# Kernel tuning notes

Measured on AMD Instinct MI355X. Metric: run time of the kernel, lower is better.

Reference implementation:

```python
import jax, jax.numpy as jnp
import numpy as np

C, A, K, S = 128, 64, 24, 4           # molecules, atoms, neighbors, species
RCR, RCA = 5.2, 3.5                   # radial / angular cutoffs (Angstrom)
ETA_R, ETA_A, ZETA = 16.0, 8.0, 32.0
LAYERS = [384, 160, 128, 96, 1]       # per-element MLP
NPAIR = S * (S + 1) // 2              # 10 unordered species pairs

_triu = np.zeros((S, S), np.int32)
_c = 0
for _i in range(S):
    for _j in range(_i, S):
        _triu[_i, _j] = _triu[_j, _i] = _c
        _c += 1
TRIU = jnp.asarray(_triu)
JJ, KK = np.triu_indices(K, 1)        # static pair-of-neighbors indices, T = K(K-1)/2


def setup_inputs() -> dict:
    key = jax.random.key(0)
    ks = jax.random.split(key, 12)
    element_idxs = jax.random.randint(ks[0], (C, A), 0, S, dtype=jnp.int32)
    neighbor_idxs = jax.random.randint(ks[1], (C, A, K), 0, A, dtype=jnp.int32)
    distances = jax.random.uniform(ks[2], (C, A, K), minval=0.8, maxval=5.0, dtype=jnp.float32)
    dirs = jax.random.normal(ks[3], (C, A, K, 3), dtype=jnp.float32)
    dirs = dirs / jnp.linalg.norm(dirs, axis=-1, keepdims=True)
    diff_vectors = dirs * distances[..., None]
    inp = {"element_idxs": element_idxs, "neighbor_idxs": neighbor_idxs,
           "distances": distances, "diff_vectors": diff_vectors}
    k = 4
    for i, (fin, fout) in enumerate(zip(LAYERS[:-1], LAYERS[1:]), 1):
        inp[f"W{i}"] = jax.random.normal(ks[k], (S, fin, fout), dtype=jnp.float32) / np.sqrt(fin).astype(np.float32); k += 1
        inp[f"b{i}"] = jax.random.normal(ks[k], (S, fout), dtype=jnp.float32) * 0.01; k += 1
    return inp


def _fc(d, rc):
    # smooth cosine cutoff, exactly zero beyond rc
    return jnp.where(d < rc, 0.5 * jnp.cos(np.float32(np.pi) * d / rc) + 0.5, 0.0)


def _celu(x, a=0.1):
    return jnp.where(x > 0, x, a * jnp.expm1(x / a))


def reference(element_idxs, neighbor_idxs, distances, diff_vectors,
              W1, b1, W2, b2, W3, b3, W4, b4):
    shfr = jnp.linspace(0.9, RCR, 17, dtype=jnp.float32)[:-1]                 # (16,)
    shfa = jnp.linspace(0.9, RCA, 5, dtype=jnp.float32)[:-1]                  # (4,)
    shfz = (jnp.arange(8, dtype=jnp.float32) + 0.5) * np.float32(np.pi / 8)   # (8,)

    # species of each neighbor: (C,A,K)
    nspec = element_idxs[jnp.arange(C)[:, None, None], neighbor_idxs]

    # ---- radial sub-AEV: (C,A,S,16) ----
    fcr = _fc(distances, RCR)
    rterm = 0.25 * jnp.exp(-ETA_R * (distances[..., None] - shfr) ** 2) * fcr[..., None]  # (C,A,K,16)
    oh_s = jax.nn.one_hot(nspec, S, dtype=rterm.dtype)                                     # (C,A,K,S)
    radial = jnp.einsum('cakr,caks->casr', rterm, oh_s).reshape(C, A, S * 16)

    # ---- angular sub-AEV over neighbor pairs (j<k): T = K(K-1)/2 ----
    d1, d2 = distances[..., JJ], distances[..., KK]                 # (C,A,T)
    v1, v2 = diff_vectors[..., JJ, :], diff_vectors[..., KK, :]      # (C,A,T,3)
    cosang = jnp.sum(v1 * v2, axis=-1) / (d1 * d2)
    ang = jnp.arccos(0.95 * cosang)                                  # torchani's 0.95 nan-guard
    f1 = ((1.0 + jnp.cos(ang[..., None] - shfz)) * 0.5) ** ZETA      # (C,A,T,8)
    f2 = jnp.exp(-ETA_A * ((d1 + d2) * 0.5)[..., None] - shfa * 0.0) if False else \
         jnp.exp(-ETA_A * (((d1 + d2) * 0.5)[..., None] - shfa) ** 2)  # (C,A,T,4)
    fc12 = _fc(d1, RCA) * _fc(d2, RCA)                               # (C,A,T)
    aterm = (2.0 * f1[..., :, None] * f2[..., None, :] * fc12[..., None, None]).reshape(C, A, JJ.size, 32)
    pidx = TRIU[nspec[..., JJ], nspec[..., KK]]                      # (C,A,T) in [0,10)
    oh_p = jax.nn.one_hot(pidx, NPAIR, dtype=aterm.dtype)            # (C,A,T,10)
    angular = jnp.einsum('catf,catp->capf', aterm, oh_p).reshape(C, A, NPAIR * 32)

    aev = jnp.concatenate([radial, angular], axis=-1)                # (C,A,384)

    # ---- per-element MLPs (computed for all species, then gathered) ----
    h = _celu(jnp.einsum('caf,sfo->caso', aev, W1) + b1)
    h = _celu(jnp.einsum('casf,sfo->caso', h, W2) + b2)
    h = _celu(jnp.einsum('casf,sfo->caso', h, W3) + b3)
    out = (jnp.einsum('casf,sfo->caso', h, W4) + b4)[..., 0]         # (C,A,S)
    atomic = jnp.take_along_axis(out, element_idxs[..., None], axis=2)[..., 0]  # (C,A)
    return atomic.sum(axis=-1)                                       # (C,) molecular energies
```

## Files before the change

kernel.cpp:

```cpp
#include <hip/hip_runtime.h>
#include <math.h>

constexpr int C_ = 128, A_ = 64, K_ = 24, S_ = 4;
constexpr int NATOM = C_ * A_;
constexpr int FAEV = 384;
constexpr float RCR = 5.2f, RCA = 3.5f;
constexpr float PI_F = 3.14159265358979323846f;
constexpr float K_A2 = -8.0f  * 1.44269504f;
constexpr float K_R2 = -64.0f * 1.44269504f;
constexpr float SQRT095 = 0.974679434f;
constexpr float SQRT2   = 1.41421356237f;

__global__ __launch_bounds__(256) void aev_kernel(const int* __restrict__ element_idxs,
                                                  const int* __restrict__ neighbor_idxs,
                                                  const float* __restrict__ distances,
                                                  const float* __restrict__ diff_vectors,
                                                  float* __restrict__ aev_out,
                                                  int* __restrict__ mol_cnt,
                                                  int* __restrict__ mol_lst,
                                                  float* __restrict__ out) {
    const int blk = blockIdx.x;
    const int c   = blk >> 4;
    const int t   = threadIdx.x;

    __shared__ int    elem_s[A_];
    __shared__ float4 u4_s[4][K_];
    __shared__ float  fcr_s[4][K_];
    __shared__ float  fca_s[4][K_];
    __shared__ int    spec_s[4][K_];
    __shared__ int    bidx_s[4][S_][K_];
    __shared__ int    nsp_s[4][S_];

    if (t < A_) elem_s[t] = element_idxs[c * A_ + t];
    __syncthreads();

    if ((blk & 15) == 0) {
        if (t < S_) {
            int n = 0;
            int* lst = mol_lst + (c * S_ + t) * A_;
            for (int a = 0; a < A_; ++a)
                if (elem_s[a] == t) lst[n++] = a;
            mol_cnt[c * S_ + t] = n;
        } else if (t == S_) {
            out[c] = 0.0f;
        }
    }

    if (t < 4 * K_) {
        int m = t / K_, k = t - m * K_;
        int base = (blk * 4 + m) * K_ + k;
        int nb = neighbor_idxs[base];
        float d = distances[base];
        float inv = __builtin_amdgcn_rcpf(d) * SQRT095;
        float4 u;
        u.x = diff_vectors[base * 3 + 0] * inv;
        u.y = diff_vectors[base * 3 + 1] * inv;
        u.z = diff_vectors[base * 3 + 2] * inv;
        u.w = 0.5f * d;
        u4_s[m][k] = u;
        spec_s[m][k] = elem_s[nb];
        fcr_s[m][k] = (d < RCR) ? (0.5f * __cosf(PI_F * d * (1.0f / RCR)) + 0.5f) : 0.0f;
        fca_s[m][k] = (d < RCA) ? (SQRT2 * (0.5f * __cosf(PI_F * d * (1.0f / RCA)) + 0.5f)) : 0.0f;
    }
    __syncthreads();

    if (t < 4 * S_) {
        int m = t >> 2, sp = t & 3, n = 0;
        #pragma unroll
        for (int k = 0; k < K_; ++k)
            if (fca_s[m][k] > 0.0f && spec_s[m][k] == sp) bidx_s[m][sp][n++] = k;
        nsp_s[m][sp] = n;
    }
    __syncthreads();

    const int m      = t >> 6;
    const int lane   = t & 63;
    const int lane32 = lane & 31;
    const int par    = lane >> 5;
    float* aev = aev_out + (size_t)(blk * 4 + m) * FAEV;

    {
        const int   spg   = lane >> 4;
        const float shfrh = 0.5f * (0.9f + 0.26875f * (float)(lane & 15));
        float acc = 0.0f;
        #pragma unroll
        for (int k = 0; k < K_; ++k) {
            float hd = u4_s[m][k].w;
            float df = hd - shfrh;
            float term = 0.25f * exp2f(df * df * K_R2) * fcr_s[m][k];
            if (spec_s[m][k] == spg) acc += term;
        }
        aev[lane] = acc;
    }

    const int zz = lane32 >> 2, yy = lane32 & 3;
    const float cz2 = 0.5f * __cosf(((float)zz + 0.5f) * (PI_F / 8.0f));
    const float sz2 = 0.5f * __sinf(((float)zz + 0.5f) * (PI_F / 8.0f));
    const float shfa_l = 0.9f + 0.65f * (float)yy;

    auto pair_term = [&](int j, int k2) -> float {
        float4 u1 = u4_s[m][j], u2 = u4_s[m][k2];
        float ca = u1.x * u2.x + u1.y * u2.y + u1.z * u2.z;
        float sa = sqrtf(1.0f - ca * ca);
        float dd = (u1.w + u2.w) - shfa_l;
        float f2 = exp2f(dd * dd * K_A2);
        float x  = 0.5f + ca * cz2 + sa * sz2;
        float x2 = x * x, x4 = x2 * x2, x8 = x4 * x4, x16 = x8 * x8;
        float tc = fca_s[m][j] * fca_s[m][k2];
        return (x16 * x16) * (f2 * tc);
    };

    #pragma unroll
    for (int spa = 0; spa < 4; ++spa) {
        #pragma unroll
        for (int spb = spa; spb < 4; ++spb) {
            const int pidx = spa * (9 - spa) / 2 + (spb - spa);
            const int na  = nsp_s[m][spa];
            const int nb2 = nsp_s[m][spb];
            float acc = 0.0f;
            if (spa == spb) {
                int jj = 0, kk = 1 + par;
                while (jj < na - 1 && kk >= na) { int ov = kk - na; ++jj; kk = jj + 1 + ov; }
                while (jj < na - 1) {
                    acc += pair_term(bidx_s[m][spa][jj], bidx_s[m][spa][kk]);
                    kk += 2;
                    while (jj < na - 1 && kk >= na) { int ov = kk - na; ++jj; kk = jj + 1 + ov; }
                }
            } else {
                int jj = 0, kk = par;
                while (jj < na && kk >= nb2) { kk -= nb2; ++jj; }
                while (jj < na) {
                    acc += pair_term(bidx_s[m][spa][jj], bidx_s[m][spb][kk]);
                    kk += 2;
                    while (jj < na && kk >= nb2) { kk -= nb2; ++jj; }
                }
            }
            float other = __shfl(acc, lane32 + 32);
            if (lane < 32) aev[64 + pidx * 32 + lane32] = acc + other;
        }
    }
}

__global__ __launch_bounds__(256) void mlp_kernel(const float* __restrict__ aev_ws,
                                                  const int* __restrict__ mol_cnt,
                                                  const int* __restrict__ mol_lst,
                                                  const float* __restrict__ W1, const float* __restrict__ b1,
                                                  const float* __restrict__ W2, const float* __restrict__ b2,
                                                  const float* __restrict__ W3, const float* __restrict__ b3,
                                                  const float* __restrict__ W4, const float* __restrict__ b4,
                                                  float* __restrict__ out) {
    const int blk   = blockIdx.x;
    const int cell  = blk / 6;
    const int tile0 = blk - cell * 6;
    const int c     = cell >> 2;
    const int s     = cell & 3;
    const int cnt   = mol_cnt[c * S_ + s];
    const int t     = threadIdx.x;

    __shared__ float aev_s[4][FAEV];
    __shared__ float h1_s[4][160];
    float (*h2_s)[128] = (float(*)[128])&aev_s[0][0];
    float (*h3_s)[96]  = (float(*)[96])(&aev_s[0][0] + 4 * 128);

    const float* W1s = W1 + s * (FAEV * 160);
    const float* b1s = b1 + s * 160;
    const float* W2s = W2 + s * (160 * 128);
    const float* b2s = b2 + s * 128;
    const float* W3s = W3 + s * (128 * 96);
    const float* b3s = b3 + s * 96;
    const float* W4s = W4 + s * 96;
    const float  bb4 = b4[s];

    for (int tile = tile0; tile * 4 < cnt; tile += 6) {
        const int base   = tile * 4;
        const int matoms = min(4, cnt - base);

        {
            int m = t >> 6, l = t & 63;
            float4* dst = (float4*)&aev_s[m][0];
            if (m < matoms) {
                int a = mol_lst[(c * S_ + s) * A_ + base + m];
                const float4* src = (const float4*)(aev_ws + (size_t)(c * A_ + a) * FAEV);
                dst[l] = src[l];
                if (l < 32) dst[l + 64] = src[l + 64];
            } else {
                dst[l] = make_float4(0.f, 0.f, 0.f, 0.f);
                if (l < 32) dst[l + 64] = make_float4(0.f, 0.f, 0.f, 0.f);
            }
        }
        __syncthreads();

        if (t < 160) {
            float acc0 = 0.f, acc1 = 0.f, acc2 = 0.f, acc3 = 0.f;
            for (int f = 0; f < FAEV; f += 4) {
                float w0 = W1s[(f + 0) * 160 + t];
                float w1 = W1s[(f + 1) * 160 + t];
                float w2 = W1s[(f + 2) * 160 + t];
                float w3 = W1s[(f + 3) * 160 + t];
                float4 a0 = *(const float4*)&aev_s[0][f];
                float4 a1 = *(const float4*)&aev_s[1][f];
                float4 a2 = *(const float4*)&aev_s[2][f];
                float4 a3 = *(const float4*)&aev_s[3][f];
                acc0 += a0.x * w0 + a0.y * w1 + a0.z * w2 + a0.w * w3;
                acc1 += a1.x * w0 + a1.y * w1 + a1.z * w2 + a1.w * w3;
                acc2 += a2.x * w0 + a2.y * w1 + a2.z * w2 + a2.w * w3;
                acc3 += a3.x * w0 + a3.y * w1 + a3.z * w2 + a3.w * w3;
            }
            float bb = b1s[t];
            float x;
            x = acc0 + bb; h1_s[0][t] = (x > 0.f) ? x : 0.1f * (__expf(10.f * x) - 1.f);
            x = acc1 + bb; h1_s[1][t] = (x > 0.f) ? x : 0.1f * (__expf(10.f * x) - 1.f);
            x = acc2 + bb; h1_s[2][t] = (x > 0.f) ? x : 0.1f * (__expf(10.f * x) - 1.f);
            x = acc3 + bb; h1_s[3][t] = (x > 0.f) ? x : 0.1f * (__expf(10.f * x) - 1.f);
        }
        __syncthreads();

        if (t < 128) {
            float acc0 = 0.f, acc1 = 0.f, acc2 = 0.f, acc3 = 0.f;
            for (int f = 0; f < 160; f += 4) {
                float w0 = W2s[(f + 0) * 128 + t];
                float w1 = W2s[(f + 1) * 128 + t];
                float w2 = W2s[(f + 2) * 128 + t];
                float w3 = W2s[(f + 3) * 128 + t];
                float4 a0 = *(const float4*)&h1_s[0][f];
                float4 a1 = *(const float4*)&h1_s[1][f];
                float4 a2 = *(const float4*)&h1_s[2][f];
                float4 a3 = *(const float4*)&h1_s[3][f];
                acc0 += a0.x * w0 + a0.y * w1 + a0.z * w2 + a0.w * w3;
                acc1 += a1.x * w0 + a1.y * w1 + a1.z * w2 + a1.w * w3;
                acc2 += a2.x * w0 + a2.y * w1 + a2.z * w2 + a2.w * w3;
                acc3 += a3.x * w0 + a3.y * w1 + a3.z * w2 + a3.w * w3;
            }
            float bb = b2s[t];
            float x;
            x = acc0 + bb; h2_s[0][t] = (x > 0.f) ? x : 0.1f * (__expf(10.f * x) - 1.f);
            x = acc1 + bb; h2_s[1][t] = (x > 0.f) ? x : 0.1f * (__expf(10.f * x) - 1.f);
            x = acc2 + bb; h2_s[2][t] = (x > 0.f) ? x : 0.1f * (__expf(10.f * x) - 1.f);
            x = acc3 + bb; h2_s[3][t] = (x > 0.f) ? x : 0.1f * (__expf(10.f * x) - 1.f);
        }
        __syncthreads();

        if (t < 96) {
            float acc0 = 0.f, acc1 = 0.f, acc2 = 0.f, acc3 = 0.f;
            for (int f = 0; f < 128; f += 4) {
                float w0 = W3s[(f + 0) * 96 + t];
                float w1 = W3s[(f + 1) * 96 + t];
                float w2 = W3s[(f + 2) * 96 + t];
                float w3 = W3s[(f + 3) * 96 + t];
                float4 a0 = *(const float4*)&h2_s[0][f];
                float4 a1 = *(const float4*)&h2_s[1][f];
                float4 a2 = *(const float4*)&h2_s[2][f];
                float4 a3 = *(const float4*)&h2_s[3][f];
                acc0 += a0.x * w0 + a0.y * w1 + a0.z * w2 + a0.w * w3;
                acc1 += a1.x * w0 + a1.y * w1 + a1.z * w2 + a1.w * w3;
                acc2 += a2.x * w0 + a2.y * w1 + a2.z * w2 + a2.w * w3;
                acc3 += a3.x * w0 + a3.y * w1 + a3.z * w2 + a3.w * w3;
            }
            float bb = b3s[t];
            float x;
            x = acc0 + bb; h3_s[0][t] = (x > 0.f) ? x : 0.1f * (__expf(10.f * x) - 1.f);
            x = acc1 + bb; h3_s[1][t] = (x > 0.f) ? x : 0.1f * (__expf(10.f * x) - 1.f);
            x = acc2 + bb; h3_s[2][t] = (x > 0.f) ? x : 0.1f * (__expf(10.f * x) - 1.f);
            x = acc3 + bb; h3_s[3][t] = (x > 0.f) ? x : 0.1f * (__expf(10.f * x) - 1.f);
        }
        __syncthreads();

        if (t < 128) {
            int m = t >> 5, l = t & 31;
            if (m < matoms) {
                float p = h3_s[m][l]      * W4s[l]
                        + h3_s[m][l + 32] * W4s[l + 32]
                        + h3_s[m][l + 64] * W4s[l + 64];
                #pragma unroll
                for (int off = 16; off >= 1; off >>= 1)
                    p += __shfl_xor(p, off, 32);
                if (l == 0) atomicAdd(&out[c], p + bb4);
            }
        }
        __syncthreads();
    }
}

extern "C" void kernel_launch(void* const* d_in, const int* in_sizes, int n_in,
                              void* d_out, int out_size, void* d_ws, size_t ws_size,
                              hipStream_t stream) {
    const int*   element_idxs  = (const int*)d_in[0];
    const int*   neighbor_idxs = (const int*)d_in[1];
    const float* distances     = (const float*)d_in[2];
    const float* diff_vectors  = (const float*)d_in[3];
    const float* W1 = (const float*)d_in[4];
    const float* b1 = (const float*)d_in[5];
    const float* W2 = (const float*)d_in[6];
    const float* b2 = (const float*)d_in[7];
    const float* W3 = (const float*)d_in[8];
    const float* b3 = (const float*)d_in[9];
    const float* W4 = (const float*)d_in[10];
    const float* b4 = (const float*)d_in[11];
    float* out = (float*)d_out;

    float* aev_ws  = (float*)d_ws;
    int*   mol_cnt = (int*)((char*)d_ws + (size_t)NATOM * FAEV * 4);
    int*   mol_lst = mol_cnt + C_ * S_;

    hipLaunchKernelGGL(aev_kernel, dim3(NATOM / 4), dim3(256), 0, stream,
                       element_idxs, neighbor_idxs, distances, diff_vectors,
                       aev_ws, mol_cnt, mol_lst, out);
    hipLaunchKernelGGL(mlp_kernel, dim3(C_ * S_ * 6), dim3(256), 0, stream,
                       aev_ws, mol_cnt, mol_lst,
                       W1, b1, W2, b2, W3, b3, W4, b4, out);
}
```

Measured before the change: 257.2 us.

## Transpose MLP weights in aev kernel and read AEV rows directly from global

The aev kernel now also writes transposed copies of W1-W3 into workspace, so each MLP output thread reads a contiguous weight row with vector loads. The MLP kernel drops shared-memory staging of AEV rows and reads them straight from global memory through wave-uniform row pointers. This aims to cut load instruction count and one barrier per tile. It adds a scattered transpose write every call and makes weight loads strided across lanes, which may reduce coalescing.

Result: slower. 291.8 us (+13.5%).

```diff
diff --git a/kernel.cpp b/kernel.cpp
--- a/kernel.cpp
+++ b/kernel.cpp
@@ -11,17 +11,45 @@
 constexpr float SQRT095 = 0.974679434f;
 constexpr float SQRT2   = 1.41421356237f;
 
+constexpr int W1N = S_ * FAEV * 160;
+constexpr int W2N = S_ * 160 * 128;
+constexpr int W3N = S_ * 128 * 96;
+constexpr int WTN = W1N + W2N + W3N;
+
 __global__ __launch_bounds__(256) void aev_kernel(const int* __restrict__ element_idxs,
                                                   const int* __restrict__ neighbor_idxs,
                                                   const float* __restrict__ distances,
                                                   const float* __restrict__ diff_vectors,
+                                                  const float* __restrict__ W1,
+                                                  const float* __restrict__ W2,
+                                                  const float* __restrict__ W3,
                                                   float* __restrict__ aev_out,
                                                   int* __restrict__ mol_cnt,
                                                   int* __restrict__ mol_lst,
+                                                  float* __restrict__ WT,
                                                   float* __restrict__ out) {
     const int blk = blockIdx.x;
     const int c   = blk >> 4;
     const int t   = threadIdx.x;
+
+    {
+        int gid = blk * 256 + t;
+        if (gid < W1N) {
+            int s = gid / (FAEV * 160), r = gid - s * (FAEV * 160);
+            int f = r / 160, o = r - f * 160;
+            WT[s * (FAEV * 160) + o * FAEV + f] = W1[gid];
+        } else if (gid < W1N + W2N) {
+            int g = gid - W1N;
+            int s = g / (160 * 128), r = g - s * (160 * 128);
+            int f = r / 128, o = r - f * 128;
+            WT[W1N + s * (160 * 128) + o * 160 + f] = W2[g];
+        } else if (gid < WTN) {
+            int g = gid - W1N - W2N;
+            int s = g / (128 * 96), r = g - s * (128 * 96);
+            int f = r / 96, o = r - f * 96;
+            WT[W1N + W2N + s * (128 * 96) + o * 128 + f] = W3[g];
+        }
+    }
 
     __shared__ int    elem_s[A_];
     __shared__ float4 u4_s[4][K_];
@@ -144,10 +172,12 @@
 __global__ __launch_bounds__(256) void mlp_kernel(const float* __restrict__ aev_ws,
                                                   const int* __restrict__ mol_cnt,
                                                   const int* __restrict__ mol_lst,
-                                                  const float* __restrict__ W1, const float* __restrict__ b1,
-                                                  const float* __restrict__ W2, const float* __restrict__ b2,
-                                                  const float* __restrict__ W3, const float* __restrict__ b3,
-                                                  const float* __restrict__ W4, const float* __restrict__ b4,
+                                                  const float* __restrict__ WT,
+                                                  const float* __restrict__ b1,
+                                                  const float* __restrict__ b2,
+                                                  const float* __restrict__ b3,
+                                                  const float* __restrict__ W4,
+                                                  const float* __restrict__ b4,
                                                   float* __restrict__ out) {
     const int blk   = blockIdx.x;
     const int cell  = blk / 6;
@@ -157,16 +187,15 @@
     const int cnt   = mol_cnt[c * S_ + s];
     const int t     = threadIdx.x;
 
-    __shared__ float aev_s[4][FAEV];
-    __shared__ float h1_s[4][160];
-    float (*h2_s)[128] = (float(*)[128])&aev_s[0][0];
-    float (*h3_s)[96]  = (float(*)[96])(&aev_s[0][0] + 4 * 128);
-
-    const float* W1s = W1 + s * (FAEV * 160);
+    __shared__ __attribute__((aligned(16))) float h1_s[4][160];
+    __shared__ __attribute__((aligned(16))) float h2_s[4][128];
+    __shared__ __attribute__((aligned(16))) float h3_s[4][96];
+
+    const float* W1T = WT + s * (FAEV * 160);
+    const float* W2T = WT + W1N + s * (160 * 128);
+    const float* W3T = WT + W1N + W2N + s * (128 * 96);
     const float* b1s = b1 + s * 160;
-    const float* W2s = W2 + s * (160 * 128);
     const float* b2s = b2 + s * 128;
-    const float* W3s = W3 + s * (128 * 96);
     const float* b3s = b3 + s * 96;
     const float* W4s = W4 + s * 96;
     const float  bb4 = b4[s];
@@ -175,36 +204,38 @@
         const int base   = tile * 4;
         const int matoms = min(4, cnt - base);
 
+        const float* row0;
+        const float* row1;
+        const float* row2;
+        const float* row3;
         {
-            int m = t >> 6, l = t & 63;
-            float4* dst = (float4*)&aev_s[m][0];
-            if (m < matoms) {
-                int a = mol_lst[(c * S_ + s) * A_ + base + m];
-                const float4* src = (const float4*)(aev_ws + (size_t)(c * A_ + a) * FAEV);
-                dst[l] = src[l];
-                if (l < 32) dst[l + 64] = src[l + 64];
-            } else {
-                dst[l] = make_float4(0.f, 0.f, 0.f, 0.f);
-                if (l < 32) dst[l + 64] = make_float4(0.f, 0.f, 0.f, 0.f);
-            }
-        }
-        __syncthreads();
+            int i0 = base + 0, i1 = min(base + 1, cnt - 1),
+                i2 = min(base + 2, cnt - 1), i3 = min(base + 3, cnt - 1);
+            const int* lst = mol_lst + (c * S_ + s) * A_;
+            int a0 = __builtin_amdgcn_readfirstlane(lst[i0]);
+            int a1 = __builtin_amdgcn_readfirstlane(lst[i1]);
+            int a2 = __builtin_amdgcn_readfirstlane(lst[i2]);
+            int a3 = __builtin_amdgcn_readfirstlane(lst[i3]);
+            row0 = aev_ws + (size_t)(c * A_ + a0) * FAEV;
+            row1 = aev_ws + (size_t)(c * A_ + a1) * FAEV;
+            row2 = aev_ws + (size_t)(c * A_ + a2) * FAEV;
+            row3 = aev_ws + (size_t)(c * A_ + a3) * FAEV;
+        }
 
         if (t < 160) {
+            const float* w = W1T + t * FAEV;
             float acc0 = 0.f, acc1 = 0.f, acc2 = 0.f, acc3 = 0.f;
+            #pragma unroll 8
             for (int f = 0; f < FAEV; f += 4) {
-                float w0 = W1s[(f + 0) * 160 + t];
-                float w1 = W1s[(f + 1) * 160 + t];
-                float w2 = W1s[(f + 2) * 160 + t];
-                float w3 = W1s[(f + 3) * 160 + t];
-                float4 a0 = *(const float4*)&aev_s[0][f];
-                float4 a1 = *(const float4*)&aev_s[1][f];
-                float4 a2 = *(const float4*)&aev_s[2][f];
-                float4 a3 = *(const float4*)&aev_s[3][f];
-                acc0 += a0.x * w0 + a0.y * w1 + a0.z * w2 + a0.w * w3;
-                acc1 += a1.x * w0 + a1.y * w1 + a1.z * w2 + a1.w * w3;
-                acc2 += a2.x * w0 + a2.y * w1 + a2.z * w2 + a2.w * w3;
-                acc3 += a3.x * w0 + a3.y * w1 + a3.z * w2 + a3.w * w3;
+                float4 wv = *(const float4*)(w + f);
+                float4 a0 = *(const float4*)(row0 + f);
+                float4 a1 = *(const float4*)(row1 + f);
+                float4 a2 = *(const float4*)(row2 + f);
+                float4 a3 = *(const float4*)(row3 + f);
+                acc0 += a0.x * wv.x + a0.y * wv.y + a0.z * wv.z + a0.w * wv.w;
+                acc1 += a1.x * wv.x + a1.y * wv.y + a1.z * wv.z + a1.w * wv.w;
+                acc2 += a2.x * wv.x + a2.y * wv.y + a2.z * wv.z + a2.w * wv.w;
+                acc3 += a3.x * wv.x + a3.y * wv.y + a3.z * wv.z + a3.w * wv.w;
             }
             float bb = b1s[t];
             float x;
@@ -216,20 +247,19 @@
         __syncthreads();
 
         if (t < 128) {
+            const float* w = W2T + t * 160;
             float acc0 = 0.f, acc1 = 0.f, acc2 = 0.f, acc3 = 0.f;
+            #pragma unroll 8
             for (int f = 0; f < 160; f += 4) {
-                float w0 = W2s[(f + 0) * 128 + t];
-                float w1 = W2s[(f + 1) * 128 + t];
-                float w2 = W2s[(f + 2) * 128 + t];
-                float w3 = W2s[(f + 3) * 128 + t];
+                float4 wv = *(const float4*)(w + f);
                 float4 a0 = *(const float4*)&h1_s[0][f];
                 float4 a1 = *(const float4*)&h1_s[1][f];
                 float4 a2 = *(const float4*)&h1_s[2][f];
                 float4 a3 = *(const float4*)&h1_s[3][f];
-                acc0 += a0.x * w0 + a0.y * w1 + a0.z * w2 + a0.w * w3;
-                acc1 += a1.x * w0 + a1.y * w1 + a1.z * w2 + a1.w * w3;
-                acc2 += a2.x * w0 + a2.y * w1 + a2.z * w2 + a2.w * w3;
-                acc3 += a3.x * w0 + a3.y * w1 + a3.z * w2 + a3.w * w3;
+                acc0 += a0.x * wv.x + a0.y * wv.y + a0.z * wv.z + a0.w * wv.w;
+                acc1 += a1.x * wv.x + a1.y * wv.y + a1.z * wv.z + a1.w * wv.w;
+                acc2 += a2.x * wv.x + a2.y * wv.y + a2.z * wv.z + a2.w * wv.w;
+                acc3 += a3.x * wv.x + a3.y * wv.y + a3.z * wv.z + a3.w * wv.w;
             }
             float bb = b2s[t];
             float x;
@@ -241,20 +271,19 @@
         __syncthreads();
 
         if (t < 96) {
+            const float* w = W3T + t * 128;
             float acc0 = 0.f, acc1 = 0.f, acc2 = 0.f, acc3 = 0.f;
+            #pragma unroll 8
             for (int f = 0; f < 128; f += 4) {
-                float w0 = W3s[(f + 0) * 96 + t];
-                float w1 = W3s[(f + 1) * 96 + t];
-                float w2 = W3s[(f + 2) * 96 + t];
-                float w3 = W3s[(f + 3) * 96 + t];
+                float4 wv = *(const float4*)(w + f);
                 float4 a0 = *(const float4*)&h2_s[0][f];
                 float4 a1 = *(const float4*)&h2_s[1][f];
                 float4 a2 = *(const float4*)&h2_s[2][f];
                 float4 a3 = *(const float4*)&h2_s[3][f];
-                acc0 += a0.x * w0 + a0.y * w1 + a0.z * w2 + a0.w * w3;
-                acc1 += a1.x * w0 + a1.y * w1 + a1.z * w2 + a1.w * w3;
-                acc2 += a2.x * w0 + a2.y * w1 + a2.z * w2 + a2.w * w3;
-                acc3 += a3.x * w0 + a3.y * w1 + a3.z * w2 + a3.w * w3;
+                acc0 += a0.x * wv.x + a0.y * wv.y + a0.z * wv.z + a0.w * wv.w;
+                acc1 += a1.x * wv.x + a1.y * wv.y + a1.z * wv.z + a1.w * wv.w;
+                acc2 += a2.x * wv.x + a2.y * wv.y + a2.z * wv.z + a2.w * wv.w;
+                acc3 += a3.x * wv.x + a3.y * wv.y + a3.z * wv.z + a3.w * wv.w;
             }
             float bb = b3s[t];
             float x;
@@ -301,11 +330,11 @@
     float* aev_ws  = (float*)d_ws;
     int*   mol_cnt = (int*)((char*)d_ws + (size_t)NATOM * FAEV * 4);
     int*   mol_lst = mol_cnt + C_ * S_;
+    float* WT      = (float*)(mol_lst + C_ * S_ * A_);
 
     hipLaunchKernelGGL(aev_kernel, dim3(NATOM / 4), dim3(256), 0, stream,
                        element_idxs, neighbor_idxs, distances, diff_vectors,
-                       aev_ws, mol_cnt, mol_lst, out);
+                       W1, W2, W3, aev_ws, mol_cnt, mol_lst, WT, out);
     hipLaunchKernelGGL(mlp_kernel, dim3(C_ * S_ * 6), dim3(256), 0, stream,
-                       aev_ws, mol_cnt, mol_lst,
-                       W1, b1, W2, b2, W3, b3, W4, b4, out);
+                       aev_ws, mol_cnt, mol_lst, WT, b1, b2, b3, W4, b4, out);
 }
```
